# Kernel optimization log

Hardware: AMD Instinct MI355X
Metric: run time of the kernel (lower is better)

Reference implementation:

```python
import jax, jax.numpy as jnp
import numpy as np

N = 50000        # nodes
E_RAND = 800000  # random edges (plus N self-loops)
NFEAT = 128
NHID = 64
NCLASS = 64
NHEADS = 8
ALPHA = 0.2      # leaky_relu negative slope


def setup_inputs() -> dict:
    key = jax.random.key(0)
    ks = jax.random.split(key, 7)
    x = jax.random.normal(ks[0], (N, NFEAT), jnp.float32)
    src = jax.random.randint(ks[1], (E_RAND,), 0, N, dtype=jnp.int32)
    dst = jax.random.randint(ks[2], (E_RAND,), 0, N, dtype=jnp.int32)
    loops = jnp.arange(N, dtype=jnp.int32)  # self-loops so every row has mass
    edge_index = jnp.stack([jnp.concatenate([src, loops]),
                            jnp.concatenate([dst, loops])], axis=0)  # [2, E]
    W1 = jax.random.normal(ks[3], (NHEADS, NFEAT, NHID), jnp.float32) / np.sqrt(NFEAT).astype(np.float32)
    a1 = jax.random.normal(ks[4], (NHEADS, 2 * NHID), jnp.float32) * 0.1
    W2 = jax.random.normal(ks[5], (NHEADS, NHID * NHEADS, NCLASS // NHEADS), jnp.float32) / np.sqrt(NHID * NHEADS).astype(np.float32)
    a2 = jax.random.normal(ks[6], (NHEADS, 2 * (NCLASS // NHEADS)), jnp.float32) * 0.1
    return {"x": x, "edge_index": edge_index, "W1": W1, "a1": a1, "W2": W2, "a2": a2}


def _sp_gat_head(x, src, dst, W, a):
    # SpGraphAttentionLayer (concat=True), eval mode (no dropout).
    h = x @ W                          # [N, F]
    F = h.shape[1]
    # a . [h_src || h_dst] decomposed into per-node terms (avoids [E, 2F] concat)
    s_src = h @ a[:F]                  # [N]
    s_dst = h @ a[F:]                  # [N]
    z = s_src[src] + s_dst[dst]        # [E] edge scores
    e = jnp.exp(-jax.nn.leaky_relu(z, ALPHA))  # [E] unnormalized attention
    n = h.shape[0]
    rowsum = jax.ops.segment_sum(e, src, num_segments=n)                      # [N]
    num = jax.ops.segment_sum(e[:, None] * h[dst], src, num_segments=n)       # [N, F]
    return jax.nn.elu(num / rowsum[:, None])


def reference(x, edge_index, W1, a1, W2, a2):
    src, dst = edge_index[0], edge_index[1]
    # layer 1: heads concat along feature dim -> [N, NHID*NHEADS]
    h1 = jnp.concatenate([_sp_gat_head(x, src, dst, W1[i], a1[i]) for i in range(NHEADS)], axis=1)
    # layer 2: heads concat -> [N, NCLASS]
    h2 = jnp.concatenate([_sp_gat_head(h1, src, dst, W2[i], a2[i]) for i in range(NHEADS)], axis=1)
    return h2
```

## Files before the change

### kernel.cpp

```cpp
#include <hip/hip_runtime.h>
#include <math.h>

typedef unsigned int u32;
typedef unsigned short u16;
typedef __attribute__((ext_vector_type(8))) short bf16x8;
typedef __attribute__((ext_vector_type(4))) float f32x4;
typedef __attribute__((ext_vector_type(2))) float f32x2;

static constexpr int TNFEAT  = 128;
static constexpr int TNHEADS = 8;
static constexpr int C1      = 512;
static constexpr int C2      = 64;

__device__ inline float bf2f(u16 u) {
  union { u32 i; float f; } c; c.i = ((u32)u) << 16; return c.f;
}
__device__ inline float bitsf(u32 u) {
  union { u32 i; float f; } c; c.i = u; return c.f;
}
__device__ inline u16 f2bf(float f) {
  union { float f; u32 i; } c; c.f = f;
  u32 r = c.i + 0x7FFF + ((c.i >> 16) & 1);
  return (u16)(r >> 16);
}
__device__ inline u32 cvt_pk_bf16(float lo, float hi) {
  u32 r;
  asm volatile("v_cvt_pk_bf16_f32 %0, %1, %2" : "=v"(r) : "v"(lo), "v"(hi));
  return r;
}
__device__ inline uint4 ld16(const u16* base, u32 byteoff) {
  return *reinterpret_cast<const uint4*>(reinterpret_cast<const char*>(base) + byteoff);
}
__device__ inline f32x2 up2(u32 q) {
  f32x2 p;
  p.x = bitsf(q << 16);
  p.y = bitsf(q & 0xffff0000u);
  return p;
}
__device__ inline float elu_fast(float v) {
  return v > 0.f ? v : (__expf(v) - 1.f);
}
__device__ inline int rdl_i(int v, int l) { return __builtin_amdgcn_readlane(v, l); }
__device__ inline float rdl_f(float v, int l) {
  union { float f; int i; } c; c.f = v;
  union { int i; float f; } d; d.i = __builtin_amdgcn_readlane(c.i, l);
  return d.f;
}

__global__ void k_zero(int* __restrict__ p, int n) {
  int i = blockIdx.x * blockDim.x + threadIdx.x;
  if (i < n) p[i] = 0;
}

__global__ void k_hist(const int* __restrict__ src, int* __restrict__ deg, int E) {
  int i = blockIdx.x * blockDim.x + threadIdx.x;
  if (i < E) atomicAdd(&deg[src[i]], 1);
}

__global__ __launch_bounds__(1024) void k_bscan1(const int* __restrict__ deg,
                                                 int* __restrict__ loc,
                                                 int* __restrict__ bsum, int n) {
  __shared__ int sdata[1024];
  int t = threadIdx.x;
  int i = blockIdx.x * 1024 + t;
  int v = (i < n) ? deg[i] : 0;
  sdata[t] = v;
  __syncthreads();
  for (int ofs = 1; ofs < 1024; ofs <<= 1) {
    int tv = (t >= ofs) ? sdata[t - ofs] : 0;
    __syncthreads();
    sdata[t] += tv;
    __syncthreads();
  }
  if (i < n) loc[i] = sdata[t];
  if (t == 1023) bsum[blockIdx.x] = sdata[1023];
}

__global__ void k_bscan2(int* __restrict__ bsum, int nb) {
  int t = threadIdx.x;
  int v = (t < nb) ? bsum[t] : 0;
  #pragma unroll
  for (int ofs = 1; ofs < 64; ofs <<= 1) {
    int u = __shfl_up(v, ofs);
    if (t >= ofs) v += u;
  }
  if (t < nb) bsum[t] = v;
}

__global__ __launch_bounds__(1024) void k_offs(const int* __restrict__ loc,
                                               const int* __restrict__ bsum,
                                               const int* __restrict__ deg,
                                               int* __restrict__ offs,
                                               int* __restrict__ cur, int n) {
  int b = blockIdx.x;
  int i = b * 1024 + threadIdx.x;
  int base = (b > 0) ? bsum[b - 1] : 0;
  if (i < n) {
    int v = base + loc[i];
    offs[i + 1] = v;
    cur[i] = v - deg[i];
  }
  if (i == 0) offs[0] = 0;
}

__global__ void k_fill(const int* __restrict__ src, const int* __restrict__ dst,
                       int* __restrict__ cur, int* __restrict__ adj, int E) {
  int i = blockIdx.x * blockDim.x + threadIdx.x;
  if (i < E) {
    int p = atomicAdd(&cur[src[i]], 1);
    adj[p] = dst[i];
  }
}

__global__ void k_packAll(const float* __restrict__ W1, const float* __restrict__ W2,
                          const float* __restrict__ a1,
                          u16* __restrict__ w1hi, u16* __restrict__ w1lo,
                          u16* __restrict__ w2hi, u16* __restrict__ w2lo,
                          u16* __restrict__ vhi, u16* __restrict__ vlo) {
  int b = blockIdx.x;
  if (b < 256) {
    int idx = b * 256 + threadIdx.x;
    int j = idx & 7, lane = (idx >> 3) & 63, ks = (idx >> 9) & 3, cg = idx >> 11;
    int col = cg * 16 + (lane & 15);
    int k = ks * 32 + (lane >> 4) * 8 + j;
    float f = W1[((size_t)(col >> 6) * 128 + k) * 64 + (col & 63)];
    u16 h = f2bf(f);
    w1hi[idx] = h;
    w1lo[idx] = f2bf(f - bf2f(h));
  } else if (b < 384) {
    int idx = (b - 256) * 256 + threadIdx.x;
    int j = idx & 7, lane = (idx >> 3) & 63, ks = (idx >> 9) & 15, cg = idx >> 13;
    int col = cg * 16 + (lane & 15);
    int k = ks * 32 + (lane >> 4) * 8 + j;
    float f = W2[((size_t)(col >> 3) * 512 + k) * 8 + (col & 7)];
    u16 h = f2bf(f);
    w2hi[idx] = h;
    w2lo[idx] = f2bf(f - bf2f(h));
  } else {
    int idx = (b - 384) * 256 + threadIdx.x;
    int j = idx & 7, lane = (idx >> 3) & 63, ks = idx >> 9;
    int k = ks * 32 + (lane >> 4) * 8 + j;
    int c = lane & 15;
    int h = c >> 1, s = c & 1;
    const float* wrow = W1 + ((size_t)h * 128 + k) * 64;
    const float* av = a1 + h * 128 + s * 64;
    float dot = 0.f;
    #pragma unroll 8
    for (int f = 0; f < 64; f++) dot = fmaf(wrow[f], av[f], dot);
    u16 hb = f2bf(dot);
    vhi[idx] = hb;
    vlo[idx] = f2bf(dot - bf2f(hb));
  }
}

__global__ __launch_bounds__(256) void k_xprep(const float* __restrict__ x,
        const u16* __restrict__ vhi, const u16* __restrict__ vlo,
        u16* __restrict__ xb, float* __restrict__ ss, float* __restrict__ sd, int N) {
  int w = threadIdx.x >> 6, lane = threadIdx.x & 63;
  int lr = lane & 15, lk = lane >> 4;
  int row0 = blockIdx.x * 64 + w * 16;
  f32x4 acc = {0.f, 0.f, 0.f, 0.f};
  for (int ks = 0; ks < 4; ++ks) {
    int row = row0 + lr;
    int rc = row < N ? row : 0;
    const float* ap = x + (size_t)rc * 128 + ks * 32 + lk * 8;
    float4 f0 = *reinterpret_cast<const float4*>(ap);
    float4 f1 = *reinterpret_cast<const float4*>(ap + 4);
    float fa[8] = {f0.x, f0.y, f0.z, f0.w, f1.x, f1.y, f1.z, f1.w};
    union { u32 u[4]; bf16x8 v; uint4 q; } ch, cl;
    #pragma unroll
    for (int p = 0; p < 4; ++p) {
      float e0 = fa[2 * p], e1 = fa[2 * p + 1];
      u32 h = cvt_pk_bf16(e0, e1);
      ch.u[p] = h;
      cl.u[p] = cvt_pk_bf16(e0 - bitsf(h << 16), e1 - bitsf(h & 0xffff0000u));
    }
    if (row < N)
      *reinterpret_cast<uint4*>(&xb[(size_t)row * 128 + ks * 32 + lk * 8]) = ch.q;
    size_t bidx = ((size_t)ks * 64 + lane) * 8;
    bf16x8 Bh = *reinterpret_cast<const bf16x8*>(&vhi[bidx]);
    bf16x8 Bl = *reinterpret_cast<const bf16x8*>(&vlo[bidx]);
    acc = __builtin_amdgcn_mfma_f32_16x16x32_bf16(ch.v, Bh, acc, 0, 0, 0);
    acc = __builtin_amdgcn_mfma_f32_16x16x32_bf16(cl.v, Bh, acc, 0, 0, 0);
    acc = __builtin_amdgcn_mfma_f32_16x16x32_bf16(ch.v, Bl, acc, 0, 0, 0);
  }
  int h = lr >> 1, s = lr & 1;
  float* dstp = (s == 0) ? ss : sd;
  #pragma unroll
  for (int r = 0; r < 4; ++r) {
    int row = row0 + lk * 4 + r;
    if (row < N) dstp[row * 8 + h] = acc[r];
  }
}

__global__ __launch_bounds__(1024, 8) void k_l12(const u16* __restrict__ xb,
        const float* __restrict__ ss, const float* __restrict__ sd,
        const int* __restrict__ offs, const int* __restrict__ adj,
        const u16* __restrict__ w1h, const u16* __restrict__ w1l,
        const u16* __restrict__ w2h, const u16* __restrict__ w2l,
        const float* __restrict__ a2,
        u16* __restrict__ h2p, float* __restrict__ ss2, float* __restrict__ sd2,
        int N) {
  __shared__ u32 g_lds[16 * 516];
  __shared__ u16 h1t[16][516];
  int wid = threadIdx.x >> 6;
  int lane = threadIdx.x & 63;
  int nodebase = blockIdx.x * 16;

  {
    int node = nodebase + wid;
    int head = lane >> 3, li = lane & 7;
    u32* gu = g_lds + wid * 516;
    if (node < N) {
      int beg = offs[node], end = offs[node + 1];
      float sS = ss[node * 8 + head];
      const char* xbb = reinterpret_cast<const char*>(xb);
      f32x2 acc2[8] = {};
      float rsum = 0.f;
      int e = beg;
      for (; e + 8 <= end; e += 8) {
        int dl = adj[e + li];
        float z = sS + sd[(u32)dl * 8u + head];
        float w = __expf(-(z > 0.f ? z : 0.2f * z));
        rsum += w;
        u32 qv[8];
        #pragma unroll
        for (int i = 0; i < 8; i++) {
          u32 di = (u32)rdl_i(dl, i);
          qv[i] = *reinterpret_cast<const u32*>(xbb + di * 256u + lane * 4u);
        }
        #pragma unroll
        for (int i = 0; i < 8; i++) {
          f32x2 xv = up2(qv[i]);
          #pragma unroll
          for (int h2 = 0; h2 < 8; h2++) {
            float wi = rdl_f(w, h2 * 8 + i);
            acc2[h2] += (f32x2){wi, wi} * xv;
          }
        }
      }
      if (e < end) {
        int m = end - e;
        int lic = li < m ? li : m - 1;
        int dl = adj[e + lic];
        float z = sS + sd[(u32)dl * 8u + head];
        float w = __expf(-(z > 0.f ? z : 0.2f * z));
        if (li >= m) w = 0.f;
        rsum += w;
        u32 qv[8];
        #pragma unroll
        for (int i = 0; i < 8; i++) {
          if (i < m) {
            u32 di = (u32)rdl_i(dl, i);
            qv[i] = *reinterpret_cast<const u32*>(xbb + di * 256u + lane * 4u);
          }
        }
        #pragma unroll
        for (int i = 0; i < 8; i++) {
          if (i < m) {
            f32x2 xv = up2(qv[i]);
            #pragma unroll
            for (int h2 = 0; h2 < 8; h2++) {
              float wi = rdl_f(w, h2 * 8 + i);
              acc2[h2] += (f32x2){wi, wi} * xv;
            }
          }
        }
      }
      rsum += __shfl_xor(rsum, 1);
      rsum += __shfl_xor(rsum, 2);
      rsum += __shfl_xor(rsum, 4);
      float inv = 1.f / rsum;
      #pragma unroll
      for (int h2 = 0; h2 < 8; h2++) {
        float ih = rdl_f(inv, h2 * 8);
        gu[h2 * 64 + lane] = cvt_pk_bf16(acc2[h2].x * ih, acc2[h2].y * ih);
      }
    } else {
      #pragma unroll
      for (int h2 = 0; h2 < 8; h2++) gu[h2 * 64 + lane] = 0;
    }
  }
  __syncthreads();

  {
    int headA = wid >> 1;
    int cf0 = (wid & 1) * 2;
    int lr = lane & 15, lk = lane >> 4;
    f32x4 acc[2] = {};
    const char* gb = reinterpret_cast<const char*>(g_lds);
    for (int ks = 0; ks < 4; ++ks) {
      bf16x8 Ah = *reinterpret_cast<const bf16x8*>(
          gb + lr * 2064 + headA * 256 + ks * 64 + lk * 16);
      #pragma unroll
      for (int c = 0; c < 2; ++c) {
        int cf = cf0 + c;
        size_t bidx = ((size_t)((headA * 4 + cf) * 4 + ks) * 64 + lane) * 8;
        bf16x8 Bh = *reinterpret_cast<const bf16x8*>(&w1h[bidx]);
        bf16x8 Bl = *reinterpret_cast<const bf16x8*>(&w1l[bidx]);
        acc[c] = __builtin_amdgcn_mfma_f32_16x16x32_bf16(Ah, Bh, acc[c], 0, 0, 0);
        acc[c] = __builtin_amdgcn_mfma_f32_16x16x32_bf16(Ah, Bl, acc[c], 0, 0, 0);
      }
    }
    #pragma unroll
    for (int r = 0; r < 4; ++r) {
      int srow = lk * 4 + r;
      #pragma unroll
      for (int c = 0; c < 2; ++c) {
        float v = elu_fast(acc[c][r]);
        h1t[srow][headA * 64 + (cf0 + c) * 16 + lr] = (u16)cvt_pk_bf16(v, v);
      }
    }
  }
  __syncthreads();

  if (wid < 4) {
    int lr = lane & 15, lk = lane >> 4;
    f32x4 acc0 = {}, acc1 = {};
    for (int ks = 0; ks < 16; ks += 2) {
      bf16x8 A0 = *reinterpret_cast<const bf16x8*>(&h1t[lr][ks * 32 + lk * 8]);
      bf16x8 A1 = *reinterpret_cast<const bf16x8*>(&h1t[lr][(ks + 1) * 32 + lk * 8]);
      size_t b0 = ((size_t)(wid * 16 + ks) * 64 + lane) * 8;
      size_t b1 = ((size_t)(wid * 16 + ks + 1) * 64 + lane) * 8;
      bf16x8 Bh0 = *reinterpret_cast<const bf16x8*>(&w2h[b0]);
      bf16x8 Bl0 = *reinterpret_cast<const bf16x8*>(&w2l[b0]);
      bf16x8 Bh1 = *reinterpret_cast<const bf16x8*>(&w2h[b1]);
      bf16x8 Bl1 = *reinterpret_cast<const bf16x8*>(&w2l[b1]);
      acc0 = __builtin_amdgcn_mfma_f32_16x16x32_bf16(A0, Bh0, acc0, 0, 0, 0);
      acc1 = __builtin_amdgcn_mfma_f32_16x16x32_bf16(A1, Bh1, acc1, 0, 0, 0);
      acc0 = __builtin_amdgcn_mfma_f32_16x16x32_bf16(A0, Bl0, acc0, 0, 0, 0);
      acc1 = __builtin_amdgcn_mfma_f32_16x16x32_bf16(A1, Bl1, acc1, 0, 0, 0);
    }
    f32x4 accB = acc0 + acc1;
    int hh2 = lr >> 3, jj = lr & 7;
    int headB = 2 * wid + hh2;
    float aS = a2[headB * 16 + jj];
    float aD = a2[headB * 16 + 8 + jj];
    #pragma unroll
    for (int r = 0; r < 4; ++r) {
      int row = nodebase + lk * 4 + r;
      float val = accB[r];
      if (row < N)
        h2p[(size_t)row * 64 + wid * 16 + lr] = (u16)cvt_pk_bf16(val, val);
      float ps = val * aS, pd = val * aD;
      ps += __shfl_xor(ps, 1); ps += __shfl_xor(ps, 2); ps += __shfl_xor(ps, 4);
      pd += __shfl_xor(pd, 1); pd += __shfl_xor(pd, 2); pd += __shfl_xor(pd, 4);
      if (jj == 0 && row < N) {
        ss2[(size_t)row * 8 + headB] = ps;
        sd2[(size_t)row * 8 + headB] = pd;
      }
    }
  }
}

__global__ __launch_bounds__(256) void k_agg2(const u16* __restrict__ H,
        const float* __restrict__ ss, const float* __restrict__ sd,
        const int* __restrict__ offs, const int* __restrict__ adj,
        float* __restrict__ outp, int n) {
  int node = (blockIdx.x * 256 + threadIdx.x) >> 6;
  int lane = threadIdx.x & 63;
  if (node >= n) return;
  int li = lane >> 3, fg = lane & 7;
  int beg = offs[node], end = offs[node + 1];
  float sS = ss[node * 8 + fg];
  f32x2 acc2[4] = {};
  float rsum = 0.f;

  auto adj2 = [&](int e, int slot) -> u32 {
    int mm = end - e; if (mm > 16) mm = 16;
    int ii = slot < mm ? slot : mm - 1;
    return (u32)adj[e + ii];
  };

  u32 d0n = 0, d1n = 0;
  if (beg + 16 < end) { d0n = adj2(beg + 16, li); d1n = adj2(beg + 16, li + 8); }
  u32 d0 = adj2(beg, li), d1 = adj2(beg, li + 8);
  uint4 rv0 = ld16(H, d0 * 128u + fg * 16u);
  uint4 rv1 = ld16(H, d1 * 128u + fg * 16u);
  float sd0 = sd[d0 * 8u + fg], sd1 = sd[d1 * 8u + fg];

  for (int e = beg; e < end; e += 16) {
    u32 d0nn = 0, d1nn = 0;
    if (e + 32 < end) { d0nn = adj2(e + 32, li); d1nn = adj2(e + 32, li + 8); }
    int mc = end - e; if (mc > 16) mc = 16;
    float z0 = sS + sd0, z1 = sS + sd1;
    float w0 = __expf(-(z0 > 0.f ? z0 : 0.2f * z0));
    float w1 = __expf(-(z1 > 0.f ? z1 : 0.2f * z1));
    w0 = li < mc ? w0 : 0.f;
    w1 = (li + 8) < mc ? w1 : 0.f;
    rsum += w0 + w1;
    bool hn = (e + 16) < end;
    uint4 rv0N = {}, rv1N = {};
    float sd0N = 0.f, sd1N = 0.f;
    if (hn) {
      rv0N = ld16(H, d0n * 128u + fg * 16u);
      rv1N = ld16(H, d1n * 128u + fg * 16u);
      sd0N = sd[d0n * 8u + fg];
      sd1N = sd[d1n * 8u + fg];
    }
    f32x2 W0 = {w0, w0}, W1v = {w1, w1};
    acc2[0] += W0 * up2(rv0.x);
    acc2[1] += W0 * up2(rv0.y);
    acc2[2] += W0 * up2(rv0.z);
    acc2[3] += W0 * up2(rv0.w);
    acc2[0] += W1v * up2(rv1.x);
    acc2[1] += W1v * up2(rv1.y);
    acc2[2] += W1v * up2(rv1.z);
    acc2[3] += W1v * up2(rv1.w);
    if (hn) { rv0 = rv0N; rv1 = rv1N; sd0 = sd0N; sd1 = sd1N; }
    d0n = d0nn; d1n = d1nn;
  }
  #pragma unroll
  for (int mask = 8; mask < 64; mask <<= 1) {
    rsum += __shfl_xor(rsum, mask);
    #pragma unroll
    for (int k = 0; k < 4; k++) {
      acc2[k].x += __shfl_xor(acc2[k].x, mask);
      acc2[k].y += __shfl_xor(acc2[k].y, mask);
    }
  }
  if (li == 0) {
    float inv = 1.f / rsum;
    float o[8];
    #pragma unroll
    for (int k = 0; k < 4; k++) {
      o[2 * k]     = elu_fast(acc2[k].x * inv);
      o[2 * k + 1] = elu_fast(acc2[k].y * inv);
    }
    float4* Ov = reinterpret_cast<float4*>(outp);
    Ov[(size_t)node * 16 + fg * 2]     = make_float4(o[0], o[1], o[2], o[3]);
    Ov[(size_t)node * 16 + fg * 2 + 1] = make_float4(o[4], o[5], o[6], o[7]);
  }
}

extern "C" void kernel_launch(void* const* d_in, const int* in_sizes, int n_in,
                              void* d_out, int out_size, void* d_ws, size_t ws_size,
                              hipStream_t stream) {
  const float* x  = (const float*)d_in[0];
  const int*   ei = (const int*)d_in[1];
  const float* W1 = (const float*)d_in[2];
  const float* a1 = (const float*)d_in[3];
  const float* W2 = (const float*)d_in[4];
  const float* a2 = (const float*)d_in[5];
  float* out = (float*)d_out;

  int N = in_sizes[0] / TNFEAT;
  int E = in_sizes[1] / 2;
  const int* src = ei;
  const int* dst = ei + E;
  int NB = (N + 1023) / 1024;

  char* base = (char*)d_ws;
  size_t off = 0;
  auto take = [&](size_t bytes) { char* p = base + off; off = (off + bytes + 255) & ~(size_t)255; return p; };
  u16*   xb    = (u16*)take((size_t)N * TNFEAT * 2);
  u16*   h2p   = (u16*)take((size_t)N * C2 * 2);
  u16*   w1hi  = (u16*)take(65536 * 2);
  u16*   w1lo  = (u16*)take(65536 * 2);
  u16*   w2hi  = (u16*)take(32768 * 2);
  u16*   w2lo  = (u16*)take(32768 * 2);
  u16*   vhi   = (u16*)take(2048 * 2);
  u16*   vlo   = (u16*)take(2048 * 2);
  float* s1s   = (float*)take((size_t)N * 8 * 4);
  float* s1d   = (float*)take((size_t)N * 8 * 4);
  float* s2s   = (float*)take((size_t)N * 8 * 4);
  float* s2d   = (float*)take((size_t)N * 8 * 4);
  int*   deg   = (int*)take((size_t)N * 4);
  int*   offs  = (int*)take((size_t)(N + 1) * 4);
  int*   cur   = (int*)take((size_t)N * 4);
  int*   loc   = (int*)take((size_t)N * 4);
  int*   bsum  = (int*)take(64 * 4);
  int*   adj   = (int*)take((size_t)E * 4);

  hipLaunchKernelGGL(k_zero, dim3((N + 255) / 256), dim3(256), 0, stream, deg, N);
  hipLaunchKernelGGL(k_hist, dim3((E + 255) / 256), dim3(256), 0, stream, src, deg, E);
  hipLaunchKernelGGL(k_bscan1, dim3(NB), dim3(1024), 0, stream, deg, loc, bsum, N);
  hipLaunchKernelGGL(k_bscan2, dim3(1), dim3(64), 0, stream, bsum, NB);
  hipLaunchKernelGGL(k_offs, dim3(NB), dim3(1024), 0, stream, loc, bsum, deg, offs, cur, N);
  hipLaunchKernelGGL(k_fill, dim3((E + 255) / 256), dim3(256), 0, stream, src, dst, cur, adj, E);

  hipLaunchKernelGGL(k_packAll, dim3(392), dim3(256), 0, stream,
                     W1, W2, a1, w1hi, w1lo, w2hi, w2lo, vhi, vlo);

  hipLaunchKernelGGL(k_xprep, dim3((N + 63) / 64), dim3(256), 0, stream,
                     x, vhi, vlo, xb, s1s, s1d, N);

  hipLaunchKernelGGL(k_l12, dim3((N + 15) / 16), dim3(1024), 0, stream,
                     xb, s1s, s1d, offs, adj, w1hi, w1lo, w2hi, w2lo, a2,
                     h2p, s2s, s2d, N);

  hipLaunchKernelGGL(k_agg2, dim3((N + 3) / 4), dim3(256), 0, stream,
                     h2p, s2s, s2d, offs, adj, out, N);
}
```

Measured before the change: 229.8 us.

## Sort nodes by degree so fused layer kernel blocks have balanced work

Adds a counting sort of nodes by out-degree (histogram, scan, scatter) and makes the fused layer-1/layer-2 kernel process nodes in permuted order, so the 16 waves in each block see similar edge counts. The goal is less intra-block imbalance, where one high-degree node stalls the whole block at the barrier before the MFMA stage. The cost is three extra small kernel launches with atomics, and scattered output writes and node reads, since nodes in a block are no longer contiguous.

```diff
diff --git a/kernel.cpp b/kernel.cpp
--- a/kernel.cpp
+++ b/kernel.cpp
@@ -109,6 +109,36 @@
   if (i < E) {
     int p = atomicAdd(&cur[src[i]], 1);
     adj[p] = dst[i];
+  }
+}
+
+__global__ void k_dhist(const int* __restrict__ deg, int* __restrict__ dbin, int n) {
+  int i = blockIdx.x * blockDim.x + threadIdx.x;
+  if (i < n) {
+    int d = deg[i]; if (d > 127) d = 127;
+    atomicAdd(&dbin[d], 1);
+  }
+}
+__global__ void k_dscan(const int* __restrict__ dbin, int* __restrict__ dcur) {
+  __shared__ int s[128];
+  int t = threadIdx.x;
+  s[t] = dbin[t];
+  __syncthreads();
+  for (int ofs = 1; ofs < 128; ofs <<= 1) {
+    int v = (t >= ofs) ? s[t - ofs] : 0;
+    __syncthreads();
+    s[t] += v;
+    __syncthreads();
+  }
+  dcur[t] = s[t] - dbin[t];
+}
+__global__ void k_dfill(const int* __restrict__ deg, int* __restrict__ dcur,
+                        int* __restrict__ perm, int n) {
+  int i = blockIdx.x * blockDim.x + threadIdx.x;
+  if (i < n) {
+    int d = deg[i]; if (d > 127) d = 127;
+    int p = atomicAdd(&dcur[d], 1);
+    perm[p] = i;
   }
 }
 
@@ -196,6 +226,7 @@
 __global__ __launch_bounds__(1024, 8) void k_l12(const u16* __restrict__ xb,
         const float* __restrict__ ss, const float* __restrict__ sd,
         const int* __restrict__ offs, const int* __restrict__ adj,
+        const int* __restrict__ perm,
         const u16* __restrict__ w1h, const u16* __restrict__ w1l,
         const u16* __restrict__ w2h, const u16* __restrict__ w2l,
         const float* __restrict__ a2,
@@ -203,15 +234,21 @@
         int N) {
   __shared__ u32 g_lds[16 * 516];
   __shared__ u16 h1t[16][516];
+  __shared__ int s_node[16];
   int wid = threadIdx.x >> 6;
   int lane = threadIdx.x & 63;
   int nodebase = blockIdx.x * 16;
+  if (threadIdx.x < 16) {
+    int idx = nodebase + threadIdx.x;
+    s_node[threadIdx.x] = idx < N ? perm[idx] : -1;
+  }
+  __syncthreads();
 
   {
-    int node = nodebase + wid;
+    int node = s_node[wid];
     int head = lane >> 3, li = lane & 7;
     u32* gu = g_lds + wid * 516;
-    if (node < N) {
+    if (node >= 0) {
       int beg = offs[node], end = offs[node + 1];
       float sS = ss[node * 8 + head];
       const char* xbb = reinterpret_cast<const char*>(xb);
@@ -338,14 +375,14 @@
     float aD = a2[headB * 16 + 8 + jj];
     #pragma unroll
     for (int r = 0; r < 4; ++r) {
-      int row = nodebase + lk * 4 + r;
+      int row = s_node[lk * 4 + r];
       float val = accB[r];
-      if (row < N)
+      if (row >= 0)
         h2p[(size_t)row * 64 + wid * 16 + lr] = (u16)cvt_pk_bf16(val, val);
       float ps = val * aS, pd = val * aD;
       ps += __shfl_xor(ps, 1); ps += __shfl_xor(ps, 2); ps += __shfl_xor(ps, 4);
       pd += __shfl_xor(pd, 1); pd += __shfl_xor(pd, 2); pd += __shfl_xor(pd, 4);
-      if (jj == 0 && row < N) {
+      if (jj == 0 && row >= 0) {
         ss2[(size_t)row * 8 + headB] = ps;
         sd2[(size_t)row * 8 + headB] = pd;
       }
@@ -465,20 +502,27 @@
   float* s1d   = (float*)take((size_t)N * 8 * 4);
   float* s2s   = (float*)take((size_t)N * 8 * 4);
   float* s2d   = (float*)take((size_t)N * 8 * 4);
-  int*   deg   = (int*)take((size_t)N * 4);
+  int*   deg   = (int*)take((size_t)(N + 128) * 4);
+  int*   dbin  = deg + N;
   int*   offs  = (int*)take((size_t)(N + 1) * 4);
   int*   cur   = (int*)take((size_t)N * 4);
   int*   loc   = (int*)take((size_t)N * 4);
   int*   bsum  = (int*)take(64 * 4);
+  int*   dcur  = (int*)take(128 * 4);
+  int*   perm  = (int*)take((size_t)N * 4);
   int*   adj   = (int*)take((size_t)E * 4);
 
-  hipLaunchKernelGGL(k_zero, dim3((N + 255) / 256), dim3(256), 0, stream, deg, N);
+  hipLaunchKernelGGL(k_zero, dim3((N + 128 + 255) / 256), dim3(256), 0, stream, deg, N + 128);
   hipLaunchKernelGGL(k_hist, dim3((E + 255) / 256), dim3(256), 0, stream, src, deg, E);
   hipLaunchKernelGGL(k_bscan1, dim3(NB), dim3(1024), 0, stream, deg, loc, bsum, N);
   hipLaunchKernelGGL(k_bscan2, dim3(1), dim3(64), 0, stream, bsum, NB);
   hipLaunchKernelGGL(k_offs, dim3(NB), dim3(1024), 0, stream, loc, bsum, deg, offs, cur, N);
   hipLaunchKernelGGL(k_fill, dim3((E + 255) / 256), dim3(256), 0, stream, src, dst, cur, adj, E);
 
+  hipLaunchKernelGGL(k_dhist, dim3((N + 255) / 256), dim3(256), 0, stream, deg, dbin, N);
+  hipLaunchKernelGGL(k_dscan, dim3(1), dim3(128), 0, stream, dbin, dcur);
+  hipLaunchKernelGGL(k_dfill, dim3((N + 255) / 256), dim3(256), 0, stream, deg, dcur, perm, N);
+
   hipLaunchKernelGGL(k_packAll, dim3(392), dim3(256), 0, stream,
                      W1, W2, a1, w1hi, w1lo, w2hi, w2lo, vhi, vlo);
 
@@ -486,7 +530,7 @@
                      x, vhi, vlo, xb, s1s, s1d, N);
 
   hipLaunchKernelGGL(k_l12, dim3((N + 15) / 16), dim3(1024), 0, stream,
-                     xb, s1s, s1d, offs, adj, w1hi, w1lo, w2hi, w2lo, a2,
+                     xb, s1s, s1d, offs, adj, perm, w1hi, w1lo, w2hi, w2lo, a2,
                      h2p, s2s, s2d, N);
 
   hipLaunchKernelGGL(k_agg2, dim3((N + 3) / 4), dim3(256), 0, stream,
```

Result: slower. 505.6 us (+120.0%).
